# Kernel tuning notes

Measured on AMD Instinct MI355X. Metric: run time of the kernel, lower is better.

## Reference

```python
import jax, jax.numpy as jnp
import numpy as np

DIM = 192
HEADS = 6
G = 16          # window size (ds_flag=0 dense attention)
B = 1
H_SZ = 256
W_SZ = 256
POS_DIM = 12    # (dim//4)//4
HIDDEN = 768    # 4*dim


def _ln(x, g, b, eps=1e-5):
    m = jnp.mean(x, -1, keepdims=True)
    v = jnp.var(x, -1, keepdims=True)
    return (x - m) / jnp.sqrt(v + eps) * g + b


def setup_inputs() -> dict:
    key = jax.random.key(0)
    ks = jax.random.split(key, 8)
    s = 0.05
    return {
        "x": jax.random.normal(ks[0], (B, H_SZ * W_SZ, DIM), jnp.float32),
        "gamma1": jnp.ones((DIM,), jnp.float32),
        "beta1": jnp.zeros((DIM,), jnp.float32),
        "qkv_w": jax.random.normal(ks[1], (DIM, 3 * DIM), jnp.float32) * s,
        "qkv_b": jnp.zeros((3 * DIM,), jnp.float32),
        "proj_w": jax.random.normal(ks[2], (DIM, DIM), jnp.float32) * s,
        "proj_b": jnp.zeros((DIM,), jnp.float32),
        "pos_proj_w": jax.random.normal(ks[3], (2, POS_DIM), jnp.float32) * s,
        "pos_proj_b": jnp.zeros((POS_DIM,), jnp.float32),
        "ln1_g": jnp.ones((POS_DIM,), jnp.float32),
        "ln1_b": jnp.zeros((POS_DIM,), jnp.float32),
        "pos1_w": jax.random.normal(ks[4], (POS_DIM, POS_DIM), jnp.float32) * s,
        "pos1_b": jnp.zeros((POS_DIM,), jnp.float32),
        "ln2_g": jnp.ones((POS_DIM,), jnp.float32),
        "ln2_b": jnp.zeros((POS_DIM,), jnp.float32),
        "pos2_w": jax.random.normal(ks[5], (POS_DIM, POS_DIM), jnp.float32) * s,
        "pos2_b": jnp.zeros((POS_DIM,), jnp.float32),
        "ln3_g": jnp.ones((POS_DIM,), jnp.float32),
        "ln3_b": jnp.zeros((POS_DIM,), jnp.float32),
        "pos3_w": jax.random.normal(ks[6], (POS_DIM, HEADS), jnp.float32) * s,
        "pos3_b": jnp.zeros((HEADS,), jnp.float32),
        "gamma2": jnp.ones((DIM,), jnp.float32),
        "beta2": jnp.zeros((DIM,), jnp.float32),
        "fc1_w": jax.random.normal(ks[7], (DIM, HIDDEN), jnp.float32) * s,
        "fc1_b": jnp.zeros((HIDDEN,), jnp.float32),
        "fc2_w": jax.random.normal(jax.random.fold_in(key, 9), (HIDDEN, DIM), jnp.float32) * s,
        "fc2_b": jnp.zeros((DIM,), jnp.float32),
        "H": H_SZ,
        "W": W_SZ,
    }


def reference(x, gamma1, beta1, qkv_w, qkv_b, proj_w, proj_b,
              pos_proj_w, pos_proj_b, ln1_g, ln1_b, pos1_w, pos1_b,
              ln2_g, ln2_b, pos2_w, pos2_b, ln3_g, ln3_b, pos3_w, pos3_b,
              gamma2, beta2, fc1_w, fc1_b, fc2_w, fc2_b, H, W):
    Bx, L, C = x.shape
    h = HEADS
    d = C // h
    N = G * G
    shortcut = x
    xn = _ln(x, gamma1, beta1)
    # window partition (H, W divisible by G -> no padding, attn_mask=None)
    xw = xn.reshape(Bx, H // G, G, W // G, G, C).transpose(0, 1, 3, 2, 4, 5)
    xw = xw.reshape(-1, N, C)                       # [B_, N, C]
    B_ = xw.shape[0]
    qkv = (xw @ qkv_w + qkv_b).reshape(B_, N, 3, h, d)
    q = qkv[:, :, 0].transpose(0, 2, 1, 3) * (d ** -0.5)   # [B_, h, N, d]
    k = qkv[:, :, 1].transpose(0, 2, 1, 3)
    v = qkv[:, :, 2].transpose(0, 2, 1, 3)
    attn = jnp.einsum('bhnd,bhmd->bhnm', q, k)      # [B_, h, N, N]
    # dynamic relative position bias (DynamicPosBias MLP + gather)
    r = jnp.arange(1 - G, G)
    biases = jnp.stack(jnp.meshgrid(r, r, indexing='ij')).reshape(2, -1).T.astype(x.dtype)  # [(2G-1)^2, 2]
    p = biases @ pos_proj_w + pos_proj_b
    p = jax.nn.relu(_ln(p, ln1_g, ln1_b)) @ pos1_w + pos1_b
    p = jax.nn.relu(_ln(p, ln2_g, ln2_b)) @ pos2_w + pos2_b
    p = jax.nn.relu(_ln(p, ln3_g, ln3_b)) @ pos3_w + pos3_b  # [(2G-1)^2, heads]
    c = jnp.stack(jnp.meshgrid(jnp.arange(G), jnp.arange(G), indexing='ij')).reshape(2, -1)
    rel = c[:, :, None] - c[:, None, :]             # [2, N, N]
    idx = (rel[0] + G - 1) * (2 * G - 1) + (rel[1] + G - 1)  # [N, N]
    attn = attn + p[idx].transpose(2, 0, 1)[None]   # add [1, h, N, N] bias
    attn = jax.nn.softmax(attn, axis=-1)
    out = jnp.einsum('bhnm,bhmd->bhnd', attn, v).transpose(0, 2, 1, 3).reshape(B_, N, C)
    out = out @ proj_w + proj_b
    # window reverse
    out = out.reshape(Bx, H // G, W // G, G, G, C).transpose(0, 1, 3, 2, 4, 5).reshape(Bx, L, C)
    x = shortcut + out
    y = _ln(x, gamma2, beta2)
    y = jax.nn.gelu(y @ fc1_w + fc1_b, approximate=False) @ fc2_w + fc2_b
    return x + y
```

## Files before the change

kernel.cpp:

```cpp
#include <hip/hip_runtime.h>
#include <hip/hip_bf16.h>

#define DIM 192
#define HEADS 6
#define QKV_N 576
#define HIDDEN 768
#define M_ROWS 65536

typedef unsigned short ushortT;
typedef __attribute__((ext_vector_type(8))) short short8v;
typedef __attribute__((ext_vector_type(4))) float f32x4;
typedef __attribute__((ext_vector_type(4))) unsigned int u32x4;

#define QSCALE_L2E 0.2550348649f
#define LOG2E 1.4426950408889634f

__device__ __forceinline__ float bf2f(ushortT u) {
    union { unsigned int i; float f; } c; c.i = ((unsigned int)u) << 16; return c.f;
}
__device__ __forceinline__ ushortT f2bf(float f) {
    union { float f; unsigned int i; } c; c.f = f;
    unsigned int i = c.i;
    return (ushortT)((i + 0x7fffu + ((i >> 16) & 1u)) >> 16);
}

#define GLOBAL_LOAD_LDS16(gp, lp) \
    __builtin_amdgcn_global_load_lds((const __attribute__((address_space(1))) void*)(gp), \
                                     (__attribute__((address_space(3))) void*)(lp), 16, 0, 0)

__device__ __forceinline__ void ln_relu_mm12(const float* in, const float* g, const float* b,
                                             const float* w, const float* bb, float* out, int nout) {
    float m = 0.f;
#pragma unroll
    for (int j = 0; j < 12; ++j) m += in[j];
    m *= (1.0f / 12.0f);
    float v = 0.f;
#pragma unroll
    for (int j = 0; j < 12; ++j) { float d = in[j] - m; v += d * d; }
    v *= (1.0f / 12.0f);
    float r = rsqrtf(v + 1e-5f);
    float t[12];
#pragma unroll
    for (int j = 0; j < 12; ++j) t[j] = fmaxf((in[j] - m) * r * g[j] + b[j], 0.0f);
    for (int j2 = 0; j2 < nout; ++j2) {
        float s = bb[j2];
#pragma unroll
        for (int j = 0; j < 12; ++j) s = fmaf(t[j], w[j * nout + j2], s);
        out[j2] = s;
    }
}

__global__ __launch_bounds__(256) void prep_kernel(
        const float* __restrict__ qkv_w, const float* __restrict__ proj_w,
        const float* __restrict__ fc1_w, const float* __restrict__ fc2_w,
        ushortT* __restrict__ qkv_wt, ushortT* __restrict__ proj_wt,
        ushortT* __restrict__ fc1_wt, ushortT* __restrict__ fc2_wt,
        const float* __restrict__ pw, const float* __restrict__ pb,
        const float* __restrict__ g1, const float* __restrict__ b1,
        const float* __restrict__ w1, const float* __restrict__ bb1,
        const float* __restrict__ g2, const float* __restrict__ b2,
        const float* __restrict__ w2, const float* __restrict__ bb2,
        const float* __restrict__ g3, const float* __restrict__ b3,
        const float* __restrict__ w3, const float* __restrict__ bb3,
        float* __restrict__ BTf) {
    __shared__ float tile[32][33];
    int blk = blockIdx.x;
    int t = threadIdx.x;
    if (blk < 432) {
        const float* W; ushortT* Wt; int K, N, bx, by;
        if (blk < 108)      { W = qkv_w;  Wt = qkv_wt;  K = 192; N = 576; bx = blk % 18;        by = blk / 18; }
        else if (blk < 144) { int r = blk - 108; W = proj_w; Wt = proj_wt; K = 192; N = 192; bx = r % 6;  by = r / 6; }
        else if (blk < 288) { int r = blk - 144; W = fc1_w;  Wt = fc1_wt;  K = 192; N = 768; bx = r % 24; by = r / 24; }
        else                { int r = blk - 288; W = fc2_w;  Wt = fc2_wt;  K = 768; N = 192; bx = r % 6;  by = r / 6; }
        int tx = t & 31, ty = t >> 5;
        int bX = bx * 32, bY = by * 32;
#pragma unroll
        for (int i = 0; i < 32; i += 8)
            tile[ty + i][tx] = W[(size_t)(bY + ty + i) * N + bX + tx];
        __syncthreads();
#pragma unroll
        for (int i = 0; i < 32; i += 8)
            Wt[(size_t)(bX + ty + i) * K + bY + tx] = f2bf(tile[tx][ty + i]);
    } else {
        int blk2 = blk - 432;
        int h = blk2 >> 8, q = blk2 & 255, kv = t;
        float di = (float)((q >> 4) - (kv >> 4));
        float dj = (float)((q & 15) - (kv & 15));
        float a[12], hh[12];
#pragma unroll
        for (int j = 0; j < 12; ++j) a[j] = di * pw[j] + dj * pw[12 + j] + pb[j];
        ln_relu_mm12(a, g1, b1, w1, bb1, hh, 12);
        ln_relu_mm12(hh, g2, b2, w2, bb2, a, 12);
        float m = 0.f;
#pragma unroll
        for (int j = 0; j < 12; ++j) m += a[j];
        m *= (1.0f / 12.0f);
        float v = 0.f;
#pragma unroll
        for (int j = 0; j < 12; ++j) { float d = a[j] - m; v += d * d; }
        v *= (1.0f / 12.0f);
        float r = rsqrtf(v + 1e-5f);
        float s = bb3[h];
#pragma unroll
        for (int j = 0; j < 12; ++j)
            s = fmaf(fmaxf((a[j] - m) * r * g3[j] + b3[j], 0.0f), w3[j * 6 + h], s);
        int wid = q >> 6, mf = (q >> 4) & 3, l4 = (q >> 2) & 3, rr = q & 3;
        int kc = kv >> 5, cc = kv & 31;
        int cf = (cc >> 4) & 1, l15 = cc & 15;
        int lane = l4 * 16 + l15;
        size_t off = ((size_t)((h * 8 + kc) * 32 + wid * 8 + mf * 2 + cf)) * 256 + lane * 4 + rr;
        BTf[off] = s * LOG2E;
    }
}

__global__ __launch_bounds__(256) void ln_kernel(const float* __restrict__ x,
                                                 const float* __restrict__ g,
                                                 const float* __restrict__ b,
                                                 ushortT* __restrict__ out) {
    int lane = threadIdx.x & 63;
    size_t row = (size_t)blockIdx.x * 4 + (threadIdx.x >> 6);
    const float* xr = x + row * DIM;
    float v0 = xr[lane], v1 = xr[lane + 64], v2 = xr[lane + 128];
    float s = v0 + v1 + v2;
    float ss = v0 * v0 + v1 * v1 + v2 * v2;
#pragma unroll
    for (int off = 32; off > 0; off >>= 1) {
        s += __shfl_xor(s, off);
        ss += __shfl_xor(ss, off);
    }
    float mean = s * (1.0f / DIM);
    float rstd = rsqrtf(ss * (1.0f / DIM) - mean * mean + 1e-5f);
    ushortT* o = out + row * DIM;
    o[lane]       = f2bf((v0 - mean) * rstd * g[lane]       + b[lane]);
    o[lane + 64]  = f2bf((v1 - mean) * rstd * g[lane + 64]  + b[lane + 64]);
    o[lane + 128] = f2bf((v2 - mean) * rstd * g[lane + 128] + b[lane + 128]);
}

template <int MODE, int NY, int KK>
__global__ __launch_bounds__(256) void mfma_gemm(const ushortT* __restrict__ A,
                                                 const ushortT* __restrict__ Wt,
                                                 const float* __restrict__ bias,
                                                 const float* __restrict__ resid,
                                                 void* __restrict__ outp,
                                                 int N) {
    __shared__ ushortT As[2][128 * 64];
    __shared__ ushortT Bs[2][64 * 64];
    const int NT = KK / 64;
    int tid = threadIdx.x;
    int lane = tid & 63, wid = tid >> 6;
    int l15 = lane & 15, l4 = lane >> 4;
    int wr = wid >> 1, wc = wid & 1;
    int p = blockIdx.x;
    int cpx = gridDim.x >> 3;
    int logical = (p & 7) * cpx + (p >> 3);
    int bx = logical / NY;
    int by = logical - bx * NY;
    int bm = bx * 128, bn = by * 64;

    f32x4 acc[4][2];
#pragma unroll
    for (int mf = 0; mf < 4; ++mf)
#pragma unroll
        for (int nf = 0; nf < 2; ++nf)
#pragma unroll
            for (int r = 0; r < 4; ++r) acc[mf][nf][r] = 0.f;

    int srow = tid >> 3;
    int schunk = (tid & 7) ^ (srow & 7);
    const ushortT* agp = A + (size_t)(bm + srow) * KK + schunk * 8;
    const ushortT* bgp = Wt + (size_t)(bn + srow) * KK + schunk * 8;

    auto STAGE = [&](int buf, int t) {
        int k0 = t * 64;
#pragma unroll
        for (int i = 0; i < 4; ++i)
            GLOBAL_LOAD_LDS16(agp + (size_t)i * 32 * KK + k0, &As[buf][i * 2048 + wid * 512]);
#pragma unroll
        for (int i = 0; i < 2; ++i)
            GLOBAL_LOAD_LDS16(bgp + (size_t)i * 32 * KK + k0, &Bs[buf][i * 2048 + wid * 512]);
    };

    STAGE(0, 0);
    for (int t = 0; t < NT; ++t) {
        int cur = t & 1;
        if (t + 1 < NT) {
            STAGE(cur ^ 1, t + 1);
            asm volatile("s_waitcnt vmcnt(6)" ::: "memory");
        } else {
            asm volatile("s_waitcnt vmcnt(0)" ::: "memory");
        }
        __builtin_amdgcn_s_barrier();
        const ushortT* Asc = As[cur];
        const ushortT* Bsc = Bs[cur];
#pragma unroll
        for (int ks = 0; ks < 2; ++ks) {
            short8v af[4], bf[2];
#pragma unroll
            for (int mf = 0; mf < 4; ++mf) {
                int row = wr * 64 + mf * 16 + l15;
                af[mf] = *(const short8v*)&Asc[row * 64 + (((ks * 4 + l4) ^ (l15 & 7)) << 3)];
            }
#pragma unroll
            for (int nf = 0; nf < 2; ++nf) {
                int row = wc * 32 + nf * 16 + l15;
                bf[nf] = *(const short8v*)&Bsc[row * 64 + (((ks * 4 + l4) ^ (l15 & 7)) << 3)];
            }
#pragma unroll
            for (int mf = 0; mf < 4; ++mf)
#pragma unroll
                for (int nf = 0; nf < 2; ++nf)
                    acc[mf][nf] = __builtin_amdgcn_mfma_f32_16x16x32_bf16(af[mf], bf[nf], acc[mf][nf], 0, 0, 0);
        }
        __builtin_amdgcn_s_barrier();
    }
#pragma unroll
    for (int mf = 0; mf < 4; ++mf) {
        size_t row = (size_t)bm + wr * 64 + mf * 16 + l4 * 4;
#pragma unroll
        for (int nf = 0; nf < 2; ++nf) {
            int col = bn + wc * 32 + nf * 16 + l15;
            float bv = bias[col];
#pragma unroll
            for (int r = 0; r < 4; ++r) {
                size_t off = (row + r) * (size_t)N + col;
                float v = acc[mf][nf][r] + bv;
                if (MODE == 0) {
                    if (col < 192) v *= QSCALE_L2E;
                    ((ushortT*)outp)[off] = f2bf(v);
                } else if (MODE == 1) {
                    float x3 = v * v * v;
                    float z = fmaf(x3, -0.1029537917f, v * -2.302205077f);
                    float e = exp2f(z);
                    v = v * __builtin_amdgcn_rcpf(1.0f + e);
                    ((ushortT*)outp)[off] = f2bf(v);
                } else if (MODE == 2) {
                    ((float*)outp)[off] = resid[off] + v;
                } else {
                    ((float*)outp)[off] += v;
                }
            }
        }
    }
}

__global__ __launch_bounds__(256, 4) void attn_mfma_kernel(const ushortT* __restrict__ qkv,
                                                           const float* __restrict__ BTf,
                                                           ushortT* __restrict__ O) {
    __shared__ ushortT Vt[32][264];
    __shared__ unsigned int Ps[4][64][20];
    int wh = blockIdx.x;
    int w = wh / 6, h = wh - w * 6;
    int wi = w >> 4, wj = w & 15;
    int tid = threadIdx.x, lane = tid & 63, wid = tid >> 6;
    int l15 = lane & 15, l4 = lane >> 4;

    {
        int t = tid;
        int pcol = (t & ~31) | (((t & 15) << 1) | ((t >> 4) & 1));
        size_t gr = (size_t)((wi * 16 + (t >> 4)) * 256 + wj * 16 + (t & 15));
        const ushortT* vp = qkv + gr * 576 + 384 + h * 32;
#pragma unroll
        for (int d0 = 0; d0 < 32; d0 += 8) {
            short8v u = *(const short8v*)(vp + d0);
#pragma unroll
            for (int j = 0; j < 8; ++j) Vt[d0 + j][pcol] = (ushortT)u[j];
        }
    }
    short8v qf[4];
    int qbase = wid * 64;
#pragma unroll
    for (int mf = 0; mf < 4; ++mf) {
        int q = qbase + mf * 16 + l15;
        size_t gr = (size_t)((wi * 16 + (q >> 4)) * 256 + wj * 16 + (q & 15));
        qf[mf] = *(const short8v*)(qkv + gr * 576 + h * 32 + l4 * 8);
    }
    __syncthreads();

    float l_run[4][4];
    f32x4 accO[4][2];
#pragma unroll
    for (int mf = 0; mf < 4; ++mf)
#pragma unroll
        for (int r = 0; r < 4; ++r) {
            l_run[mf][r] = 0.f;
            accO[mf][0][r] = 0.f;
            accO[mf][1][r] = 0.f;
        }
    const float* btb = BTf + ((size_t)(h * 8) * 32 + wid * 8) * 256 + lane * 4;

    for (int kc = 0; kc < 8; ++kc) {
        short8v kf[2];
#pragma unroll
        for (int cf = 0; cf < 2; ++cf) {
            int kv = kc * 32 + cf * 16 + l15;
            size_t gr = (size_t)((wi * 16 + (kv >> 4)) * 256 + wj * 16 + (kv & 15));
            kf[cf] = *(const short8v*)(qkv + gr * 576 + 192 + h * 32 + l4 * 8);
        }
        short8v vb[2];
#pragma unroll
        for (int nf = 0; nf < 2; ++nf)
            vb[nf] = *(const short8v*)&Vt[nf * 16 + l15][kc * 32 + l4 * 8];
#pragma unroll
        for (int mf = 0; mf < 4; ++mf) {
            f32x4 s0 = *(const f32x4*)(btb + (size_t)(kc * 32 + mf * 2 + 0) * 256);
            f32x4 s1 = *(const f32x4*)(btb + (size_t)(kc * 32 + mf * 2 + 1) * 256);
            __builtin_amdgcn_s_setprio(1);
            s0 = __builtin_amdgcn_mfma_f32_16x16x32_bf16(qf[mf], kf[0], s0, 0, 0, 0);
            s1 = __builtin_amdgcn_mfma_f32_16x16x32_bf16(qf[mf], kf[1], s1, 0, 0, 0);
            __builtin_amdgcn_s_setprio(0);
#pragma unroll
            for (int r = 0; r < 4; ++r) {
                float p0 = exp2f(s0[r]);
                float p1 = exp2f(s1[r]);
                l_run[mf][r] += p0 + p1;
                unsigned int pk;
                asm("v_cvt_pk_bf16_f32 %0, %1, %2" : "=v"(pk) : "v"(p0), "v"(p1));
                Ps[wid][mf * 16 + 4 * l4 + r][l15] = pk;
            }
            u32x4 pr = *(const u32x4*)&Ps[wid][mf * 16 + l15][l4 * 4];
            short8v pa = __builtin_bit_cast(short8v, pr);
            __builtin_amdgcn_s_setprio(1);
            accO[mf][0] = __builtin_amdgcn_mfma_f32_16x16x32_bf16(pa, vb[0], accO[mf][0], 0, 0, 0);
            accO[mf][1] = __builtin_amdgcn_mfma_f32_16x16x32_bf16(pa, vb[1], accO[mf][1], 0, 0, 0);
            __builtin_amdgcn_s_setprio(0);
        }
    }
#pragma unroll
    for (int mf = 0; mf < 4; ++mf)
#pragma unroll
        for (int r = 0; r < 4; ++r) {
            float l = l_run[mf][r];
            l += __shfl_xor(l, 1);
            l += __shfl_xor(l, 2);
            l += __shfl_xor(l, 4);
            l += __shfl_xor(l, 8);
            l_run[mf][r] = 1.0f / l;
        }
#pragma unroll
    for (int mf = 0; mf < 4; ++mf) {
        int q0 = qbase + mf * 16 + 4 * l4;
#pragma unroll
        for (int r = 0; r < 4; ++r) {
            int q = q0 + r;
            size_t gr = (size_t)((wi * 16 + (q >> 4)) * 256 + wj * 16 + (q & 15));
            ushortT* op = O + gr * 192 + h * 32 + l15;
            float inv = l_run[mf][r];
            op[0]  = f2bf(accO[mf][0][r] * inv);
            op[16] = f2bf(accO[mf][1][r] * inv);
        }
    }
}

extern "C" void kernel_launch(void* const* d_in, const int* in_sizes, int n_in,
                              void* d_out, int out_size, void* d_ws, size_t ws_size,
                              hipStream_t stream) {
    const float* x        = (const float*)d_in[0];
    const float* gamma1   = (const float*)d_in[1];
    const float* beta1    = (const float*)d_in[2];
    const float* qkv_w    = (const float*)d_in[3];
    const float* qkv_b    = (const float*)d_in[4];
    const float* proj_w   = (const float*)d_in[5];
    const float* proj_b   = (const float*)d_in[6];
    const float* pos_proj_w = (const float*)d_in[7];
    const float* pos_proj_b = (const float*)d_in[8];
    const float* ln1_g    = (const float*)d_in[9];
    const float* ln1_b    = (const float*)d_in[10];
    const float* pos1_w   = (const float*)d_in[11];
    const float* pos1_b   = (const float*)d_in[12];
    const float* ln2_g    = (const float*)d_in[13];
    const float* ln2_b    = (const float*)d_in[14];
    const float* pos2_w   = (const float*)d_in[15];
    const float* pos2_b   = (const float*)d_in[16];
    const float* ln3_g    = (const float*)d_in[17];
    const float* ln3_b    = (const float*)d_in[18];
    const float* pos3_w   = (const float*)d_in[19];
    const float* pos3_b   = (const float*)d_in[20];
    const float* gamma2   = (const float*)d_in[21];
    const float* beta2    = (const float*)d_in[22];
    const float* fc1_w    = (const float*)d_in[23];
    const float* fc1_b    = (const float*)d_in[24];
    const float* fc2_w    = (const float*)d_in[25];
    const float* fc2_b    = (const float*)d_in[26];
    float* out = (float*)d_out;

    char* ws = (char*)d_ws;
    ushortT* qkv = (ushortT*)(ws + 0);
    ushortT* y1  = (ushortT*)(ws + 0);
    ushortT* xn   = (ushortT*)(ws + 100663296);
    ushortT* Obuf = xn;
    ushortT* xn2  = xn;
    ushortT* qkv_wt  = (ushortT*)(ws + 125829120);
    ushortT* proj_wt = (ushortT*)(ws + 126050304);
    ushortT* fc1_wt  = (ushortT*)(ws + 126124032);
    ushortT* fc2_wt  = (ushortT*)(ws + 126418944);
    float*   BTf     = (float*)(ws + 126713856);

    prep_kernel<<<1968, 256, 0, stream>>>(
        qkv_w, proj_w, fc1_w, fc2_w, qkv_wt, proj_wt, fc1_wt, fc2_wt,
        pos_proj_w, pos_proj_b, ln1_g, ln1_b, pos1_w, pos1_b,
        ln2_g, ln2_b, pos2_w, pos2_b, ln3_g, ln3_b, pos3_w, pos3_b, BTf);
    ln_kernel<<<M_ROWS / 4, 256, 0, stream>>>(x, gamma1, beta1, xn);
    mfma_gemm<0, 9, 192><<<(M_ROWS / 128) * (QKV_N / 64), 256, 0, stream>>>(
        xn, qkv_wt, qkv_b, nullptr, qkv, QKV_N);
    attn_mfma_kernel<<<1536, 256, 0, stream>>>(qkv, BTf, Obuf);
    mfma_gemm<2, 3, 192><<<(M_ROWS / 128) * (DIM / 64), 256, 0, stream>>>(
        Obuf, proj_wt, proj_b, x, out, DIM);
    ln_kernel<<<M_ROWS / 4, 256, 0, stream>>>(out, gamma2, beta2, xn2);
    mfma_gemm<1, 12, 192><<<(M_ROWS / 128) * (HIDDEN / 64), 256, 0, stream>>>(
        xn2, fc1_wt, fc1_b, nullptr, y1, HIDDEN);
    mfma_gemm<3, 3, 768><<<(M_ROWS / 128) * (DIM / 64), 256, 0, stream>>>(
        y1, fc2_wt, fc2_b, nullptr, out, DIM);
}
```

Baseline: 230.5 us.

## Fuse LN2, fc1+GELU and fc2 into a single MLP kernel

```diff
diff --git a/kernel.cpp b/kernel.cpp
--- a/kernel.cpp
+++ b/kernel.cpp
@@ -22,6 +22,12 @@
     union { float f; unsigned int i; } c; c.f = f;
     unsigned int i = c.i;
     return (ushortT)((i + 0x7fffu + ((i >> 16) & 1u)) >> 16);
+}
+__device__ __forceinline__ float fast_gelu(float v) {
+    float x3 = v * v * v;
+    float z = fmaf(x3, -0.1029537917f, v * -2.302205077f);
+    float e = exp2f(z);
+    return v * __builtin_amdgcn_rcpf(1.0f + e);
 }
 
 #define GLOBAL_LOAD_LDS16(gp, lp) \
@@ -67,20 +73,21 @@
     int blk = blockIdx.x;
     int t = threadIdx.x;
     if (blk < 432) {
-        const float* W; ushortT* Wt; int K, N, bx, by;
+        const float* W; ushortT* Wt; int K, N, bx, by; bool perm = false;
         if (blk < 108)      { W = qkv_w;  Wt = qkv_wt;  K = 192; N = 576; bx = blk % 18;        by = blk / 18; }
         else if (blk < 144) { int r = blk - 108; W = proj_w; Wt = proj_wt; K = 192; N = 192; bx = r % 6;  by = r / 6; }
         else if (blk < 288) { int r = blk - 144; W = fc1_w;  Wt = fc1_wt;  K = 192; N = 768; bx = r % 24; by = r / 24; }
-        else                { int r = blk - 288; W = fc2_w;  Wt = fc2_wt;  K = 768; N = 192; bx = r % 6;  by = r / 6; }
+        else                { int r = blk - 288; W = fc2_w;  Wt = fc2_wt;  K = 768; N = 192; bx = r % 6;  by = r / 6; perm = true; }
         int tx = t & 31, ty = t >> 5;
         int bX = bx * 32, bY = by * 32;
 #pragma unroll
         for (int i = 0; i < 32; i += 8)
             tile[ty + i][tx] = W[(size_t)(bY + ty + i) * N + bX + tx];
         __syncthreads();
+        int kcol = perm ? (((tx & 15) << 1) | (tx >> 4)) : tx;
 #pragma unroll
         for (int i = 0; i < 32; i += 8)
-            Wt[(size_t)(bX + ty + i) * K + bY + tx] = f2bf(tile[tx][ty + i]);
+            Wt[(size_t)(bX + ty + i) * K + bY + kcol] = f2bf(tile[tx][ty + i]);
     } else {
         int blk2 = blk - 432;
         int h = blk2 >> 8, q = blk2 & 255, kv = t;
@@ -227,18 +234,141 @@
                 if (MODE == 0) {
                     if (col < 192) v *= QSCALE_L2E;
                     ((ushortT*)outp)[off] = f2bf(v);
-                } else if (MODE == 1) {
-                    float x3 = v * v * v;
-                    float z = fmaf(x3, -0.1029537917f, v * -2.302205077f);
-                    float e = exp2f(z);
-                    v = v * __builtin_amdgcn_rcpf(1.0f + e);
-                    ((ushortT*)outp)[off] = f2bf(v);
-                } else if (MODE == 2) {
+                } else {
                     ((float*)outp)[off] = resid[off] + v;
-                } else {
-                    ((float*)outp)[off] += v;
                 }
             }
+        }
+    }
+}
+
+__global__ __launch_bounds__(256, 2) void mlp_kernel(float* out,
+                                                     const ushortT* __restrict__ fc1t,
+                                                     const ushortT* __restrict__ fc2t,
+                                                     const float* __restrict__ fc1b,
+                                                     const float* __restrict__ fc2b,
+                                                     const float* __restrict__ g,
+                                                     const float* __restrict__ b) {
+    __shared__ ushortT As[64 * 192];
+    __shared__ ushortT Bs1[64 * 192];
+    __shared__ ushortT Bs2[192 * 64];
+    __shared__ unsigned int Yl[4][16 * 32];
+    int tid = threadIdx.x, lane = tid & 63, wid = tid >> 6;
+    int l15 = lane & 15, l4 = lane >> 4;
+    size_t bm = (size_t)blockIdx.x * 64;
+
+    {
+        int row = tid >> 2, part = tid & 3;
+        const float* xr = out + (bm + row) * 192 + part * 48;
+        float v[48];
+        float s = 0.f, ss = 0.f;
+#pragma unroll
+        for (int i = 0; i < 48; ++i) { v[i] = xr[i]; s += v[i]; ss += v[i] * v[i]; }
+        s += __shfl_xor(s, 1); ss += __shfl_xor(ss, 1);
+        s += __shfl_xor(s, 2); ss += __shfl_xor(ss, 2);
+        float mean = s * (1.0f / 192.0f);
+        float rstd = rsqrtf(ss * (1.0f / 192.0f) - mean * mean + 1e-5f);
+#pragma unroll
+        for (int c = 0; c < 6; ++c) {
+            int chunk = part * 6 + c;
+            int kt = chunk >> 3, w = chunk & 7;
+            int wp = w ^ (row & 7);
+            short8v pk8;
+#pragma unroll
+            for (int j = 0; j < 8; ++j) {
+                int col = part * 48 + c * 8 + j;
+                float nv = (v[c * 8 + j] - mean) * rstd * g[col] + b[col];
+                pk8[j] = (short)f2bf(nv);
+            }
+            *(short8v*)&As[row * 192 + kt * 64 + wp * 8] = pk8;
+        }
+    }
+    int aoff1[6], aoff2[6];
+#pragma unroll
+    for (int i = 0; i < 6; ++i) {
+        int u = tid + i * 256;
+        int r1 = u / 24, rem = u - r1 * 24;
+        int kt = rem >> 3, wp = rem & 7;
+        aoff1[i] = r1 * 192 + kt * 64 + ((wp ^ (r1 & 7)) << 3);
+        int r2 = u >> 3, wp2 = u & 7;
+        aoff2[i] = r2 * 768 + ((wp2 ^ (r2 & 7)) << 3);
+    }
+    __syncthreads();
+
+    f32x4 accO[12];
+#pragma unroll
+    for (int nf = 0; nf < 12; ++nf)
+#pragma unroll
+        for (int r = 0; r < 4; ++r) accO[nf][r] = 0.f;
+
+    int arow = wid * 16 + l15;
+    for (int hc = 0; hc < 12; ++hc) {
+#pragma unroll
+        for (int i = 0; i < 6; ++i)
+            GLOBAL_LOAD_LDS16(fc1t + hc * 12288 + aoff1[i], &Bs1[(wid * 64 + i * 256) * 8]);
+#pragma unroll
+        for (int i = 0; i < 6; ++i)
+            GLOBAL_LOAD_LDS16(fc2t + hc * 64 + aoff2[i], &Bs2[(wid * 64 + i * 256) * 8]);
+        asm volatile("s_waitcnt vmcnt(0)" ::: "memory");
+        __builtin_amdgcn_s_barrier();
+        f32x4 ya[4];
+#pragma unroll
+        for (int n = 0; n < 4; ++n) {
+            float bv = fc1b[hc * 64 + n * 16 + l15];
+            ya[n][0] = bv; ya[n][1] = bv; ya[n][2] = bv; ya[n][3] = bv;
+        }
+        __builtin_amdgcn_s_setprio(1);
+#pragma unroll
+        for (int kt = 0; kt < 3; ++kt)
+#pragma unroll
+            for (int ks = 0; ks < 2; ++ks) {
+                int wp = ((ks * 4 + l4) ^ (l15 & 7)) << 3;
+                short8v af = *(const short8v*)&As[arow * 192 + kt * 64 + wp];
+#pragma unroll
+                for (int n = 0; n < 4; ++n) {
+                    short8v bf = *(const short8v*)&Bs1[(n * 16 + l15) * 192 + kt * 64 + wp];
+                    ya[n] = __builtin_amdgcn_mfma_f32_16x16x32_bf16(af, bf, ya[n], 0, 0, 0);
+                }
+            }
+        __builtin_amdgcn_s_setprio(0);
+#pragma unroll
+        for (int r = 0; r < 4; ++r) {
+            int row = 4 * l4 + r;
+            int key = row & 7;
+#pragma unroll
+            for (int gg = 0; gg < 2; ++gg) {
+                float y0 = fast_gelu(ya[gg * 2 + 0][r]);
+                float y1 = fast_gelu(ya[gg * 2 + 1][r]);
+                unsigned int pk;
+                asm("v_cvt_pk_bf16_f32 %0, %1, %2" : "=v"(pk) : "v"(y0), "v"(y1));
+                int ucol = gg * 16 + l15;
+                int ch = (ucol >> 2) ^ key;
+                Yl[wid][row * 32 + ch * 4 + (ucol & 3)] = pk;
+            }
+        }
+        __builtin_amdgcn_s_setprio(1);
+#pragma unroll
+        for (int gg = 0; gg < 2; ++gg) {
+            u32x4 pr = *(const u32x4*)&Yl[wid][l15 * 32 + (((gg * 4 + l4) ^ (l15 & 7)) << 2)];
+            short8v pa = __builtin_bit_cast(short8v, pr);
+#pragma unroll
+            for (int nf = 0; nf < 12; ++nf) {
+                short8v bf = *(const short8v*)&Bs2[(nf * 16 + l15) * 64 + (((gg * 4 + l4) ^ (l15 & 7)) << 3)];
+                accO[nf] = __builtin_amdgcn_mfma_f32_16x16x32_bf16(pa, bf, accO[nf], 0, 0, 0);
+            }
+        }
+        __builtin_amdgcn_s_setprio(0);
+        __builtin_amdgcn_s_barrier();
+    }
+    size_t row0 = bm + wid * 16 + l4 * 4;
+#pragma unroll
+    for (int nf = 0; nf < 12; ++nf) {
+        int col = nf * 16 + l15;
+        float bv = fc2b[col];
+#pragma unroll
+        for (int r = 0; r < 4; ++r) {
+            size_t off = (row0 + r) * 192 + col;
+            out[off] = out[off] + bv + accO[nf][r];
         }
     }
 }
@@ -385,10 +515,8 @@
 
     char* ws = (char*)d_ws;
     ushortT* qkv = (ushortT*)(ws + 0);
-    ushortT* y1  = (ushortT*)(ws + 0);
     ushortT* xn   = (ushortT*)(ws + 100663296);
     ushortT* Obuf = xn;
-    ushortT* xn2  = xn;
     ushortT* qkv_wt  = (ushortT*)(ws + 125829120);
     ushortT* proj_wt = (ushortT*)(ws + 126050304);
     ushortT* fc1_wt  = (ushortT*)(ws + 126124032);
@@ -405,9 +533,6 @@
     attn_mfma_kernel<<<1536, 256, 0, stream>>>(qkv, BTf, Obuf);
     mfma_gemm<2, 3, 192><<<(M_ROWS / 128) * (DIM / 64), 256, 0, stream>>>(
         Obuf, proj_wt, proj_b, x, out, DIM);
-    ln_kernel<<<M_ROWS / 4, 256, 0, stream>>>(out, gamma2, beta2, xn2);
-    mfma_gemm<1, 12, 192><<<(M_ROWS / 128) * (HIDDEN / 64), 256, 0, stream>>>(
-        xn2, fc1_wt, fc1_b, nullptr, y1, HIDDEN);
-    mfma_gemm<3, 3, 768><<<(M_ROWS / 128) * (DIM / 64), 256, 0, stream>>>(
-        y1, fc2_wt, fc2_b, nullptr, out, DIM);
-}
+    mlp_kernel<<<M_ROWS / 64, 256, 0, stream>>>(
+        out, fc1_wt, fc2_wt, fc1_b, fc2_b, gamma2, beta2);
+}
```

Measured after the change: 216.5 us. 6.1% less time.
